# Optimization experiments

Measured on AMD Instinct MI355X. Metric: run time of the kernel, lower is better.

The kernel has to match this reference:

```python
import jax, jax.numpy as jnp
import numpy as np

B, LQ, LK = 8, 256, 256
Q_SIZE = K_SIZE = H = D_V = 256
MASK_VALUE = -1000000.0


def setup_inputs() -> dict:
    key = jax.random.key(0)
    kq, kk, kv, kl, kwq, kwk, kwv = jax.random.split(key, 7)
    # Linear weights, torch nn.Linear stores (out, in); init ~ U(-1/sqrt(in), 1/sqrt(in))
    def lin(k, out_f, in_f):
        bound = 1.0 / np.sqrt(in_f)
        return jax.random.uniform(k, (out_f, in_f), jnp.float32, -bound, bound)
    return {
        "queries": jax.random.normal(kq, (B, LQ, Q_SIZE), jnp.float32),
        "keyes": jax.random.normal(kk, (B, LK, K_SIZE), jnp.float32),
        "values": jax.random.normal(kv, (B, LK, D_V), jnp.float32),
        "valid_lens": jax.random.randint(kl, (B,), 1, LK + 1),
        "W_q": lin(kwq, H, Q_SIZE),
        "W_k": lin(kwk, H, K_SIZE),
        "W_v": lin(kwv, 1, H),
    }


def reference(queries, keyes, values, valid_lens, W_q, W_k, W_v):
    # Projections (nn.Linear without bias): x @ W.T
    q = jnp.einsum("bqd,hd->bqh", queries, W_q)            # (B, Lq, H)
    k = jnp.einsum("bkd,hd->bkh", keyes, W_k)              # (B, Lk, H)
    # Broadcast-add + tanh: (B, Lq, Lk, H)
    features = jnp.tanh(q[:, :, None, :] + k[:, None, :, :])
    # W_v reduction H -> 1, squeeze: scores (B, Lq, Lk)
    scores = jnp.einsum("bqkh,h->bqk", features, W_v[0])
    # sequence_mask over the last (key) axis with value -1e6
    lk = scores.shape[-1]
    mask = jnp.arange(lk)[None, None, :] < valid_lens[:, None, None]  # (B,1,Lk)
    scores = jnp.where(mask, scores, MASK_VALUE)
    # NOTE: this repo's masked_softmax normalizes over dim=1 (the query axis),
    # faithfully reproduced here.
    attention_weights = jax.nn.softmax(scores, axis=1)
    # dropout is identity in eval / p=0.0
    return jnp.einsum("bqk,bkd->bqd", attention_weights, values)
```

## Files before the change

kernel.cpp:

```cpp
#include <hip/hip_runtime.h>

typedef float vf4 __attribute__((ext_vector_type(4)));
typedef float vf2 __attribute__((ext_vector_type(2)));

#define LOG2E 1.4426950408889634f
#define TWO_LOG2E 2.8853900817779268f

__device__ __forceinline__ float fexp2(float x) { return __builtin_amdgcn_exp2f(x); }
__device__ __forceinline__ float frcp(float x) { return __builtin_amdgcn_rcpf(x); }

__global__ __launch_bounds__(256) void proj_kernel(
    const float* __restrict__ queries, const float* __restrict__ keyes,
    const float* __restrict__ Wq, const float* __restrict__ Wk,
    float* __restrict__ QpH, float* __restrict__ KpH,
    float* __restrict__ Rsum) {
  __shared__ alignas(16) float At[16 * 68];
  __shared__ alignas(16) float Bt[16 * 68];
  const int t = threadIdx.x;
  if (blockIdx.x == 0 && blockIdx.y == 0 && blockIdx.z == 0) {
    *(vf4*)&Rsum[t * 8] = (vf4){0.f, 0.f, 0.f, 0.f};
    *(vf4*)&Rsum[t * 8 + 4] = (vf4){0.f, 0.f, 0.f, 0.f};
  }
  const int m0 = blockIdx.x * 64;
  const int n0 = blockIdx.y * 64;
  const int k0 = blockIdx.z * 128;
  const bool isQ = (m0 < 2048);
  const float* X = isQ ? queries : keyes;
  const float* W = isQ ? Wq : Wk;
  float* C = (isQ ? QpH : KpH) + blockIdx.z * 524288;
  const int mb = isQ ? m0 : (m0 - 2048);

  const int lm = t >> 2;
  const int lq = t & 3;
  const int mm4 = (t & 15) * 4;
  const int nn4 = (t >> 4) * 4;

  float acc[4][4] = {};
  for (int kc = k0; kc < k0 + 128; kc += 16) {
    __syncthreads();
    vf4 xa = *(const vf4*)&X[(mb + lm) * 256 + kc + lq * 4];
    vf4 wb = *(const vf4*)&W[(n0 + lm) * 256 + kc + lq * 4];
#pragma unroll
    for (int c = 0; c < 4; ++c) {
      At[(lq * 4 + c) * 68 + lm] = xa[c];
      Bt[(lq * 4 + c) * 68 + lm] = wb[c];
    }
    __syncthreads();
#pragma unroll
    for (int kk = 0; kk < 16; ++kk) {
      vf4 a4 = *(const vf4*)&At[kk * 68 + mm4];
      vf4 b4 = *(const vf4*)&Bt[kk * 68 + nn4];
#pragma unroll
      for (int i = 0; i < 4; ++i)
#pragma unroll
        for (int j = 0; j < 4; ++j) acc[i][j] += a4[i] * b4[j];
    }
  }
#pragma unroll
  for (int i = 0; i < 4; ++i) {
    vf4 o = {fexp2(acc[i][0] * TWO_LOG2E), fexp2(acc[i][1] * TWO_LOG2E),
             fexp2(acc[i][2] * TWO_LOG2E), fexp2(acc[i][3] * TWO_LOG2E)};
    *(vf4*)&C[(mb + mm4 + i) * 256 + n0 + nn4] = o;
  }
}

__global__ __launch_bounds__(256) void scores_exp_kernel(
    const float* __restrict__ QpH, const float* __restrict__ KpH,
    const float* __restrict__ Wv, const int* __restrict__ valid_lens,
    float* __restrict__ E, float* __restrict__ Rsum) {
  __shared__ alignas(16) float Qs[32 * 32];
  __shared__ alignas(16) float Ks[32 * 32];
  const int t = threadIdx.x;
  const int i0 = blockIdx.x * 32;
  const int j0 = blockIdx.y * 32;
  const int b = blockIdx.z;
  const int ti = t & 15;
  const int tj = t >> 4;

  float Swv;
  {
    vf4 w4 = *(const vf4*)&Wv[(t & 63) * 4];
    float sw = w4[0] + w4[1] + w4[2] + w4[3];
#pragma unroll
    for (int off = 1; off < 64; off <<= 1) sw += __shfl_xor(sw, off, 64);
    Swv = sw;
  }

  const int srow = t >> 3;
  const int scg = t & 7;
  const int swcol = ((scg ^ (srow & 7)) << 2);
  const int qxor = ti & 7;
  const int kxor = tj & 7;

  float acc[2][2] = {};
  for (int hc = 0; hc < 8; ++hc) {
    __syncthreads();
    const int qoff = (((b << 8) + i0 + srow) << 8) + hc * 32 + scg * 4;
    const int koff = (((b << 8) + j0 + srow) << 8) + hc * 32 + scg * 4;
    vf4 qv = *(const vf4*)&QpH[qoff];
    vf4 qv2 = *(const vf4*)&QpH[524288 + qoff];
    vf4 kv = *(const vf4*)&KpH[koff];
    vf4 kv2 = *(const vf4*)&KpH[524288 + koff];
    *(vf4*)&Qs[srow * 32 + swcol] = qv * qv2;
    *(vf4*)&Ks[srow * 32 + swcol] = kv * kv2;
    __syncthreads();
#pragma unroll
    for (int hh = 0; hh < 8; ++hh) {
      vf4 q0 = *(const vf4*)&Qs[ti * 32 + ((hh ^ qxor) << 2)];
      vf4 q1 = *(const vf4*)&Qs[(ti + 16) * 32 + ((hh ^ qxor) << 2)];
      vf4 k0 = *(const vf4*)&Ks[tj * 32 + ((hh ^ kxor) << 2)];
      vf4 k1 = *(const vf4*)&Ks[(tj + 16) * 32 + ((hh ^ kxor) << 2)];
      const int hb = hc * 32 + hh * 4;
      const float w0 = Wv[hb + 0];
      const float w1 = Wv[hb + 1];
      const float w2 = Wv[hb + 2];
      const float w3 = Wv[hb + 3];
      auto term = [&](const vf4& q, const vf4& k, float& a) {
        float A0 = __builtin_fmaf(q[0], k[0], 1.0f);
        float A1 = __builtin_fmaf(q[1], k[1], 1.0f);
        float A2 = __builtin_fmaf(q[2], k[2], 1.0f);
        float A3 = __builtin_fmaf(q[3], k[3], 1.0f);
        float d01 = A0 * A1;
        float d23 = A2 * A3;
        float n01 = __builtin_fmaf(w0, A1, w1 * A0);
        float n23 = __builtin_fmaf(w2, A3, w3 * A2);
        float num = __builtin_fmaf(n01, d23, n23 * d01);
        a = __builtin_fmaf(num, frcp(d01 * d23), a);
      };
      term(q0, k0, acc[0][0]);
      term(q0, k1, acc[0][1]);
      term(q1, k0, acc[1][0]);
      term(q1, k1, acc[1][1]);
    }
  }

  const int len = valid_lens[b];
#pragma unroll
  for (int c = 0; c < 2; ++c) {
    const int j = j0 + tj + 16 * c;
    const bool masked = (j >= len);
    float ev[2];
#pragma unroll
    for (int r = 0; r < 2; ++r) {
      const int i = i0 + ti + 16 * r;
      const float score = Swv - 2.0f * acc[r][c];
      ev[r] = masked ? 1.0f : fexp2(score * LOG2E);
      E[(((b << 8) + j) << 8) + i] = ev[r];
    }
    float s = ev[0] + ev[1];
#pragma unroll
    for (int off = 1; off < 16; off <<= 1) s += __shfl_xor(s, off, 64);
    if (ti == 0) atomicAdd(&Rsum[(b << 8) + j], s);
  }
}

__global__ __launch_bounds__(256) void out_kernel(
    const float* __restrict__ E, const float* __restrict__ Rsum,
    const float* __restrict__ V, float* __restrict__ out) {
  __shared__ alignas(16) float As[32 * 36];
  __shared__ alignas(16) float Bs[32 * 68];
  const int t = threadIdx.x;
  const int i0 = blockIdx.x * 32;
  const int d0 = blockIdx.y * 64;
  const int b = blockIdx.z;
  const int ti = t & 15;
  const int td = t >> 4;
  const int sr = t >> 3;
  const int sc4 = (t & 7) * 4;

  float acc[2][4] = {};
  for (int jc = 0; jc < 8; ++jc) {
    const int jb = jc * 32;
    __syncthreads();
    const float rj = frcp(Rsum[(b << 8) + jb + sr]);
    {
      vf4 a = *(const vf4*)&E[(((b << 8) + jb + sr) << 8) + i0 + sc4];
      *(vf4*)&As[sr * 36 + sc4] = a * rj;
    }
#pragma unroll
    for (int s = 0; s < 2; ++s) {
      const int col = sc4 + s * 32;
      *(vf4*)&Bs[sr * 68 + col] =
          *(const vf4*)&V[(((b << 8) + jb + sr) << 8) + d0 + col];
    }
    __syncthreads();
#pragma unroll
    for (int j = 0; j < 32; ++j) {
      vf2 a = *(const vf2*)&As[j * 36 + 2 * ti];
      vf4 b4 = *(const vf4*)&Bs[j * 68 + td * 4];
#pragma unroll
      for (int c = 0; c < 4; ++c) {
        acc[0][c] += a[0] * b4[c];
        acc[1][c] += a[1] * b4[c];
      }
    }
  }
#pragma unroll
  for (int r = 0; r < 2; ++r) {
    vf4 o = {acc[r][0], acc[r][1], acc[r][2], acc[r][3]};
    *(vf4*)&out[(((b << 8) + i0 + 2 * ti + r) << 8) + d0 + td * 4] = o;
  }
}

extern "C" void kernel_launch(void* const* d_in, const int* in_sizes, int n_in,
                              void* d_out, int out_size, void* d_ws, size_t ws_size,
                              hipStream_t stream) {
  const float* queries = (const float*)d_in[0];
  const float* keyes = (const float*)d_in[1];
  const float* values = (const float*)d_in[2];
  const int* valid_lens = (const int*)d_in[3];
  const float* Wq = (const float*)d_in[4];
  const float* Wk = (const float*)d_in[5];
  const float* Wv = (const float*)d_in[6];
  float* out = (float*)d_out;

  float* QpH = (float*)d_ws;
  float* KpH = QpH + 2 * 524288;
  float* E = KpH + 2 * 524288;
  float* Rsum = E + 524288;

  proj_kernel<<<dim3(64, 4, 2), 256, 0, stream>>>(queries, keyes, Wq, Wk,
                                                  QpH, KpH, Rsum);
  scores_exp_kernel<<<dim3(8, 8, 8), 256, 0, stream>>>(QpH, KpH, Wv,
                                                       valid_lens, E, Rsum);
  out_kernel<<<dim3(8, 4, 8), 256, 0, stream>>>(E, Rsum, values, out);
}
```

Baseline: 106.7 us.

## Split projection K-dim four ways with 128-row tiles, multiply exp partials

The projection kernel now uses 128x64 output tiles, with each thread computing an 8x4 block, and splits the 256-long reduction into four 64-wide chunks instead of two 128-wide ones. Each chunk stores exp(2*partial), and the scores kernel multiplies the four partial exponentials to rebuild exp(2*q). This raises register reuse per thread and shortens each block's serial K loop. In exchange, the scores kernel reads twice as much workspace (four partial buffers per operand) and the workspace footprint doubles.

New measurement: 109.6 us. 1.03x slower.

```diff
diff --git a/kernel.cpp b/kernel.cpp
--- a/kernel.cpp
+++ b/kernel.cpp
@@ -14,53 +14,65 @@
     const float* __restrict__ Wq, const float* __restrict__ Wk,
     float* __restrict__ QpH, float* __restrict__ KpH,
     float* __restrict__ Rsum) {
-  __shared__ alignas(16) float At[16 * 68];
+  __shared__ alignas(16) float At[16 * 132];
   __shared__ alignas(16) float Bt[16 * 68];
   const int t = threadIdx.x;
   if (blockIdx.x == 0 && blockIdx.y == 0 && blockIdx.z == 0) {
     *(vf4*)&Rsum[t * 8] = (vf4){0.f, 0.f, 0.f, 0.f};
     *(vf4*)&Rsum[t * 8 + 4] = (vf4){0.f, 0.f, 0.f, 0.f};
   }
-  const int m0 = blockIdx.x * 64;
+  const int m0 = blockIdx.x * 128;
   const int n0 = blockIdx.y * 64;
-  const int k0 = blockIdx.z * 128;
+  const int k0 = blockIdx.z * 64;
   const bool isQ = (m0 < 2048);
   const float* X = isQ ? queries : keyes;
   const float* W = isQ ? Wq : Wk;
   float* C = (isQ ? QpH : KpH) + blockIdx.z * 524288;
   const int mb = isQ ? m0 : (m0 - 2048);
 
-  const int lm = t >> 2;
-  const int lq = t & 3;
-  const int mm4 = (t & 15) * 4;
-  const int nn4 = (t >> 4) * 4;
-
-  float acc[4][4] = {};
-  for (int kc = k0; kc < k0 + 128; kc += 16) {
-    __syncthreads();
-    vf4 xa = *(const vf4*)&X[(mb + lm) * 256 + kc + lq * 4];
-    vf4 wb = *(const vf4*)&W[(n0 + lm) * 256 + kc + lq * 4];
+  const int lmA = t >> 1;
+  const int lqA = t & 1;
+  const int lmB = t >> 2;
+  const int lqB = t & 3;
+  const int tm4 = (t & 15) * 4;
+  const int tn4 = (t >> 4) * 4;
+
+  float acc[8][4] = {};
+  for (int kc = k0; kc < k0 + 64; kc += 16) {
+    __syncthreads();
+    const float* asrc = &X[(mb + lmA) * 256 + kc + lqA * 8];
+    vf4 xa0 = *(const vf4*)asrc;
+    vf4 xa1 = *(const vf4*)(asrc + 4);
+    vf4 wb = *(const vf4*)&W[(n0 + lmB) * 256 + kc + lqB * 4];
 #pragma unroll
     for (int c = 0; c < 4; ++c) {
-      At[(lq * 4 + c) * 68 + lm] = xa[c];
-      Bt[(lq * 4 + c) * 68 + lm] = wb[c];
+      At[(lqA * 8 + c) * 132 + lmA] = xa0[c];
+      At[(lqA * 8 + 4 + c) * 132 + lmA] = xa1[c];
+      Bt[(lqB * 4 + c) * 68 + lmB] = wb[c];
     }
     __syncthreads();
 #pragma unroll
     for (int kk = 0; kk < 16; ++kk) {
-      vf4 a4 = *(const vf4*)&At[kk * 68 + mm4];
-      vf4 b4 = *(const vf4*)&Bt[kk * 68 + nn4];
+      vf4 a0 = *(const vf4*)&At[kk * 132 + tm4];
+      vf4 a1 = *(const vf4*)&At[kk * 132 + tm4 + 64];
+      vf4 b4 = *(const vf4*)&Bt[kk * 68 + tn4];
 #pragma unroll
       for (int i = 0; i < 4; ++i)
 #pragma unroll
-        for (int j = 0; j < 4; ++j) acc[i][j] += a4[i] * b4[j];
+        for (int j = 0; j < 4; ++j) {
+          acc[i][j] += a0[i] * b4[j];
+          acc[4 + i][j] += a1[i] * b4[j];
+        }
     }
   }
 #pragma unroll
   for (int i = 0; i < 4; ++i) {
-    vf4 o = {fexp2(acc[i][0] * TWO_LOG2E), fexp2(acc[i][1] * TWO_LOG2E),
-             fexp2(acc[i][2] * TWO_LOG2E), fexp2(acc[i][3] * TWO_LOG2E)};
-    *(vf4*)&C[(mb + mm4 + i) * 256 + n0 + nn4] = o;
+    vf4 o0 = {fexp2(acc[i][0] * TWO_LOG2E), fexp2(acc[i][1] * TWO_LOG2E),
+              fexp2(acc[i][2] * TWO_LOG2E), fexp2(acc[i][3] * TWO_LOG2E)};
+    *(vf4*)&C[(mb + tm4 + i) * 256 + n0 + tn4] = o0;
+    vf4 o1 = {fexp2(acc[4 + i][0] * TWO_LOG2E), fexp2(acc[4 + i][1] * TWO_LOG2E),
+              fexp2(acc[4 + i][2] * TWO_LOG2E), fexp2(acc[4 + i][3] * TWO_LOG2E)};
+    *(vf4*)&C[(mb + 64 + tm4 + i) * 256 + n0 + tn4] = o1;
   }
 }
 
@@ -97,12 +109,14 @@
     __syncthreads();
     const int qoff = (((b << 8) + i0 + srow) << 8) + hc * 32 + scg * 4;
     const int koff = (((b << 8) + j0 + srow) << 8) + hc * 32 + scg * 4;
-    vf4 qv = *(const vf4*)&QpH[qoff];
-    vf4 qv2 = *(const vf4*)&QpH[524288 + qoff];
-    vf4 kv = *(const vf4*)&KpH[koff];
-    vf4 kv2 = *(const vf4*)&KpH[524288 + koff];
-    *(vf4*)&Qs[srow * 32 + swcol] = qv * qv2;
-    *(vf4*)&Ks[srow * 32 + swcol] = kv * kv2;
+    vf4 qv = *(const vf4*)&QpH[qoff] * *(const vf4*)&QpH[524288 + qoff] *
+             *(const vf4*)&QpH[2 * 524288 + qoff] *
+             *(const vf4*)&QpH[3 * 524288 + qoff];
+    vf4 kv = *(const vf4*)&KpH[koff] * *(const vf4*)&KpH[524288 + koff] *
+             *(const vf4*)&KpH[2 * 524288 + koff] *
+             *(const vf4*)&KpH[3 * 524288 + koff];
+    *(vf4*)&Qs[srow * 32 + swcol] = qv;
+    *(vf4*)&Ks[srow * 32 + swcol] = kv;
     __syncthreads();
 #pragma unroll
     for (int hh = 0; hh < 8; ++hh) {
@@ -215,11 +229,11 @@
   float* out = (float*)d_out;
 
   float* QpH = (float*)d_ws;
-  float* KpH = QpH + 2 * 524288;
-  float* E = KpH + 2 * 524288;
+  float* KpH = QpH + 4 * 524288;
+  float* E = KpH + 4 * 524288;
   float* Rsum = E + 524288;
 
-  proj_kernel<<<dim3(64, 4, 2), 256, 0, stream>>>(queries, keyes, Wq, Wk,
+  proj_kernel<<<dim3(32, 4, 4), 256, 0, stream>>>(queries, keyes, Wq, Wk,
                                                   QpH, KpH, Rsum);
   scores_exp_kernel<<<dim3(8, 8, 8), 256, 0, stream>>>(QpH, KpH, Wv,
                                                        valid_lens, E, Rsum);
```

## Reduce split-K projection halves in shared memory instead of storing two exp buffers

Applied to the files above, without the earlier changes.

The projection kernel now runs both K halves in one 512-thread block and sums the partial accumulators through shared memory before a single exp and store. This removes the second QpH/KpH buffer and halves the global loads in the scores kernel, which no longer multiplies two exp partials. In exchange, the projection grid has half as many blocks, adds an extra barrier and LDS reduction, and leaves half the threads idle during the epilogue.

Result: no change. 107.6 us (+0.8%).

```diff
diff --git a/kernel.cpp b/kernel.cpp
--- a/kernel.cpp
+++ b/kernel.cpp
@@ -9,34 +9,36 @@
 __device__ __forceinline__ float fexp2(float x) { return __builtin_amdgcn_exp2f(x); }
 __device__ __forceinline__ float frcp(float x) { return __builtin_amdgcn_rcpf(x); }
 
-__global__ __launch_bounds__(256) void proj_kernel(
+__global__ __launch_bounds__(512) void proj_kernel(
     const float* __restrict__ queries, const float* __restrict__ keyes,
     const float* __restrict__ Wq, const float* __restrict__ Wk,
     float* __restrict__ QpH, float* __restrict__ KpH,
     float* __restrict__ Rsum) {
-  __shared__ alignas(16) float At[16 * 68];
-  __shared__ alignas(16) float Bt[16 * 68];
+  __shared__ alignas(16) float smem[4352];
   const int t = threadIdx.x;
-  if (blockIdx.x == 0 && blockIdx.y == 0 && blockIdx.z == 0) {
-    *(vf4*)&Rsum[t * 8] = (vf4){0.f, 0.f, 0.f, 0.f};
-    *(vf4*)&Rsum[t * 8 + 4] = (vf4){0.f, 0.f, 0.f, 0.f};
+  if (blockIdx.x == 0 && blockIdx.y == 0) {
+    *(vf4*)&Rsum[t * 4] = (vf4){0.f, 0.f, 0.f, 0.f};
   }
   const int m0 = blockIdx.x * 64;
   const int n0 = blockIdx.y * 64;
-  const int k0 = blockIdx.z * 128;
   const bool isQ = (m0 < 2048);
   const float* X = isQ ? queries : keyes;
   const float* W = isQ ? Wq : Wk;
-  float* C = (isQ ? QpH : KpH) + blockIdx.z * 524288;
+  float* C = isQ ? QpH : KpH;
   const int mb = isQ ? m0 : (m0 - 2048);
 
-  const int lm = t >> 2;
-  const int lq = t & 3;
-  const int mm4 = (t & 15) * 4;
-  const int nn4 = (t >> 4) * 4;
+  const int g = t >> 8;
+  const int tl = t & 255;
+  float* At = smem + g * 1088;
+  float* Bt = smem + 2176 + g * 1088;
+  const int lm = tl >> 2;
+  const int lq = tl & 3;
+  const int mm4 = (tl & 15) * 4;
+  const int nn4 = (tl >> 4) * 4;
 
   float acc[4][4] = {};
-  for (int kc = k0; kc < k0 + 128; kc += 16) {
+  const int kbase = g * 128;
+  for (int kc = kbase; kc < kbase + 128; kc += 16) {
     __syncthreads();
     vf4 xa = *(const vf4*)&X[(mb + lm) * 256 + kc + lq * 4];
     vf4 wb = *(const vf4*)&W[(n0 + lm) * 256 + kc + lq * 4];
@@ -56,11 +58,25 @@
         for (int j = 0; j < 4; ++j) acc[i][j] += a4[i] * b4[j];
     }
   }
-#pragma unroll
-  for (int i = 0; i < 4; ++i) {
-    vf4 o = {fexp2(acc[i][0] * TWO_LOG2E), fexp2(acc[i][1] * TWO_LOG2E),
-             fexp2(acc[i][2] * TWO_LOG2E), fexp2(acc[i][3] * TWO_LOG2E)};
-    *(vf4*)&C[(mb + mm4 + i) * 256 + n0 + nn4] = o;
+  __syncthreads();
+  float* red = smem;
+  if (g == 1) {
+#pragma unroll
+    for (int i = 0; i < 4; ++i)
+      *(vf4*)&red[tl * 16 + i * 4] =
+          (vf4){acc[i][0], acc[i][1], acc[i][2], acc[i][3]};
+  }
+  __syncthreads();
+  if (g == 0) {
+#pragma unroll
+    for (int i = 0; i < 4; ++i) {
+      vf4 p = *(const vf4*)&red[tl * 16 + i * 4];
+      vf4 o = {fexp2((acc[i][0] + p[0]) * TWO_LOG2E),
+               fexp2((acc[i][1] + p[1]) * TWO_LOG2E),
+               fexp2((acc[i][2] + p[2]) * TWO_LOG2E),
+               fexp2((acc[i][3] + p[3]) * TWO_LOG2E)};
+      *(vf4*)&C[(mb + mm4 + i) * 256 + n0 + nn4] = o;
+    }
   }
 }
 
@@ -97,12 +113,8 @@
     __syncthreads();
     const int qoff = (((b << 8) + i0 + srow) << 8) + hc * 32 + scg * 4;
     const int koff = (((b << 8) + j0 + srow) << 8) + hc * 32 + scg * 4;
-    vf4 qv = *(const vf4*)&QpH[qoff];
-    vf4 qv2 = *(const vf4*)&QpH[524288 + qoff];
-    vf4 kv = *(const vf4*)&KpH[koff];
-    vf4 kv2 = *(const vf4*)&KpH[524288 + koff];
-    *(vf4*)&Qs[srow * 32 + swcol] = qv * qv2;
-    *(vf4*)&Ks[srow * 32 + swcol] = kv * kv2;
+    *(vf4*)&Qs[srow * 32 + swcol] = *(const vf4*)&QpH[qoff];
+    *(vf4*)&Ks[srow * 32 + swcol] = *(const vf4*)&KpH[koff];
     __syncthreads();
 #pragma unroll
     for (int hh = 0; hh < 8; ++hh) {
@@ -215,12 +227,12 @@
   float* out = (float*)d_out;
 
   float* QpH = (float*)d_ws;
-  float* KpH = QpH + 2 * 524288;
-  float* E = KpH + 2 * 524288;
+  float* KpH = QpH + 524288;
+  float* E = KpH + 524288;
   float* Rsum = E + 524288;
 
-  proj_kernel<<<dim3(64, 4, 2), 256, 0, stream>>>(queries, keyes, Wq, Wk,
-                                                  QpH, KpH, Rsum);
+  proj_kernel<<<dim3(64, 4), 512, 0, stream>>>(queries, keyes, Wq, Wk,
+                                               QpH, KpH, Rsum);
   scores_exp_kernel<<<dim3(8, 8, 8), 256, 0, stream>>>(QpH, KpH, Wv,
                                                        valid_lens, E, Rsum);
   out_kernel<<<dim3(8, 4, 8), 256, 0, stream>>>(E, Rsum, values, out);
```

## Stage full H in LDS and merge eight tanh terms per reciprocal

Applied to the files above, without the earlier changes.

The scores kernel now loads all eight H-chunks of the Q and K products into LDS up front, with a single barrier instead of two barriers per chunk. It then combines eight rational tanh terms into one fraction, so each accumulation needs one reciprocal instead of two. This targets the barrier and transcendental-unit cost in the hot inner loop. The trade-offs are 64KB of LDS per block, which limits how many blocks fit on a CU, and larger denominator products that raise the risk of overflow on extreme inputs.

Result: no change. 107.0 us (+0.3%).

```diff
diff --git a/kernel.cpp b/kernel.cpp
--- a/kernel.cpp
+++ b/kernel.cpp
@@ -64,12 +64,12 @@
   }
 }
 
-__global__ __launch_bounds__(256) void scores_exp_kernel(
+__global__ __launch_bounds__(256, 2) void scores_exp_kernel(
     const float* __restrict__ QpH, const float* __restrict__ KpH,
     const float* __restrict__ Wv, const int* __restrict__ valid_lens,
     float* __restrict__ E, float* __restrict__ Rsum) {
-  __shared__ alignas(16) float Qs[32 * 32];
-  __shared__ alignas(16) float Ks[32 * 32];
+  __shared__ alignas(16) float Qs[8 * 32 * 32];
+  __shared__ alignas(16) float Ks[8 * 32 * 32];
   const int t = threadIdx.x;
   const int i0 = blockIdx.x * 32;
   const int j0 = blockIdx.y * 32;
@@ -92,45 +92,66 @@
   const int qxor = ti & 7;
   const int kxor = tj & 7;
 
-  float acc[2][2] = {};
+#pragma unroll
   for (int hc = 0; hc < 8; ++hc) {
-    __syncthreads();
     const int qoff = (((b << 8) + i0 + srow) << 8) + hc * 32 + scg * 4;
     const int koff = (((b << 8) + j0 + srow) << 8) + hc * 32 + scg * 4;
-    vf4 qv = *(const vf4*)&QpH[qoff];
-    vf4 qv2 = *(const vf4*)&QpH[524288 + qoff];
-    vf4 kv = *(const vf4*)&KpH[koff];
-    vf4 kv2 = *(const vf4*)&KpH[524288 + koff];
-    *(vf4*)&Qs[srow * 32 + swcol] = qv * qv2;
-    *(vf4*)&Ks[srow * 32 + swcol] = kv * kv2;
-    __syncthreads();
-#pragma unroll
-    for (int hh = 0; hh < 8; ++hh) {
-      vf4 q0 = *(const vf4*)&Qs[ti * 32 + ((hh ^ qxor) << 2)];
-      vf4 q1 = *(const vf4*)&Qs[(ti + 16) * 32 + ((hh ^ qxor) << 2)];
-      vf4 k0 = *(const vf4*)&Ks[tj * 32 + ((hh ^ kxor) << 2)];
-      vf4 k1 = *(const vf4*)&Ks[(tj + 16) * 32 + ((hh ^ kxor) << 2)];
+    vf4 qv = *(const vf4*)&QpH[qoff] * *(const vf4*)&QpH[524288 + qoff];
+    vf4 kv = *(const vf4*)&KpH[koff] * *(const vf4*)&KpH[524288 + koff];
+    *(vf4*)&Qs[hc * 1024 + srow * 32 + swcol] = qv;
+    *(vf4*)&Ks[hc * 1024 + srow * 32 + swcol] = kv;
+  }
+  __syncthreads();
+
+  float acc[2][2] = {};
+#pragma unroll 2
+  for (int hc = 0; hc < 8; ++hc) {
+    const float* Qc = &Qs[hc * 1024];
+    const float* Kc = &Ks[hc * 1024];
+#pragma unroll
+    for (int hh = 0; hh < 8; hh += 2) {
+      vf4 q0a = *(const vf4*)&Qc[ti * 32 + ((hh ^ qxor) << 2)];
+      vf4 q1a = *(const vf4*)&Qc[(ti + 16) * 32 + ((hh ^ qxor) << 2)];
+      vf4 k0a = *(const vf4*)&Kc[tj * 32 + ((hh ^ kxor) << 2)];
+      vf4 k1a = *(const vf4*)&Kc[(tj + 16) * 32 + ((hh ^ kxor) << 2)];
+      vf4 q0b = *(const vf4*)&Qc[ti * 32 + (((hh + 1) ^ qxor) << 2)];
+      vf4 q1b = *(const vf4*)&Qc[(ti + 16) * 32 + (((hh + 1) ^ qxor) << 2)];
+      vf4 k0b = *(const vf4*)&Kc[tj * 32 + (((hh + 1) ^ kxor) << 2)];
+      vf4 k1b = *(const vf4*)&Kc[(tj + 16) * 32 + (((hh + 1) ^ kxor) << 2)];
       const int hb = hc * 32 + hh * 4;
       const float w0 = Wv[hb + 0];
       const float w1 = Wv[hb + 1];
       const float w2 = Wv[hb + 2];
       const float w3 = Wv[hb + 3];
-      auto term = [&](const vf4& q, const vf4& k, float& a) {
-        float A0 = __builtin_fmaf(q[0], k[0], 1.0f);
-        float A1 = __builtin_fmaf(q[1], k[1], 1.0f);
-        float A2 = __builtin_fmaf(q[2], k[2], 1.0f);
-        float A3 = __builtin_fmaf(q[3], k[3], 1.0f);
-        float d01 = A0 * A1;
-        float d23 = A2 * A3;
+      const float w4 = Wv[hb + 4];
+      const float w5 = Wv[hb + 5];
+      const float w6 = Wv[hb + 6];
+      const float w7 = Wv[hb + 7];
+      auto term8 = [&](const vf4& qa, const vf4& ka, const vf4& qb,
+                       const vf4& kb, float& a) {
+        float A0 = __builtin_fmaf(qa[0], ka[0], 1.0f);
+        float A1 = __builtin_fmaf(qa[1], ka[1], 1.0f);
+        float A2 = __builtin_fmaf(qa[2], ka[2], 1.0f);
+        float A3 = __builtin_fmaf(qa[3], ka[3], 1.0f);
+        float A4 = __builtin_fmaf(qb[0], kb[0], 1.0f);
+        float A5 = __builtin_fmaf(qb[1], kb[1], 1.0f);
+        float A6 = __builtin_fmaf(qb[2], kb[2], 1.0f);
+        float A7 = __builtin_fmaf(qb[3], kb[3], 1.0f);
+        float d01 = A0 * A1, d23 = A2 * A3, d45 = A4 * A5, d67 = A6 * A7;
         float n01 = __builtin_fmaf(w0, A1, w1 * A0);
         float n23 = __builtin_fmaf(w2, A3, w3 * A2);
-        float num = __builtin_fmaf(n01, d23, n23 * d01);
-        a = __builtin_fmaf(num, frcp(d01 * d23), a);
+        float n45 = __builtin_fmaf(w4, A5, w5 * A4);
+        float n67 = __builtin_fmaf(w6, A7, w7 * A6);
+        float da = d01 * d23, db = d45 * d67;
+        float na = __builtin_fmaf(n01, d23, n23 * d01);
+        float nb = __builtin_fmaf(n45, d67, n67 * d45);
+        float num = __builtin_fmaf(na, db, nb * da);
+        a = __builtin_fmaf(num, frcp(da * db), a);
       };
-      term(q0, k0, acc[0][0]);
-      term(q0, k1, acc[0][1]);
-      term(q1, k0, acc[1][0]);
-      term(q1, k1, acc[1][1]);
+      term8(q0a, k0a, q0b, k0b, acc[0][0]);
+      term8(q0a, k1a, q0b, k1b, acc[0][1]);
+      term8(q1a, k0a, q1b, k0b, acc[1][0]);
+      term8(q1a, k1a, q1b, k1b, acc[1][1]);
     }
   }
 
```
